# Kernel tuning notes

Measured on AMD Instinct MI355X. Metric: run time of the kernel, lower is better.

Reference implementation:

```python
import jax, jax.numpy as jnp
import numpy as np

N_STEPS = 3000  # hardcoded in the original forward loop


def setup_inputs() -> dict:
    return {
        "starting_value": jnp.float32(0.0),
        "rate": jnp.float32(1.0),
        "non_decision_time": jnp.float32(0.0),
        "threshold": jnp.float32(1.0),
        "noise": jnp.float32(1.0),
        "time_step_size": jnp.float32(0.01),
        "num_walkers": 1048576,
    }


def reference(starting_value, rate, non_decision_time, threshold, noise,
              time_step_size, num_walkers):
    # torch.normal(mean=rate*dt*active, std=noise*active):
    # inactive walkers get std=0, mean=0 -> dw == 0 exactly.
    # Equivalent: dw = active * (rate*dt + noise * z), z ~ N(0,1).
    sqrt_dt = jnp.sqrt(time_step_size)
    particle0 = jnp.zeros((num_walkers,), jnp.float32) + starting_value
    rts0 = jnp.zeros((num_walkers,), jnp.float32)
    active0 = jnp.ones((num_walkers,), jnp.bool_)

    keys = jax.random.split(jax.random.key(0), N_STEPS)

    def step(carry, k):
        particle, rts, active = carry
        a = active.astype(jnp.float32)
        z = jax.random.normal(k, (num_walkers,), jnp.float32)
        dw = (rate * time_step_size + noise * z) * a
        particle = particle + dw * sqrt_dt
        rts = rts + a
        active = jnp.abs(particle) < threshold
        return (particle, rts, active), None

    (particle, rts, _), _ = jax.lax.scan(step, (particle0, rts0, active0), keys)

    rts = non_decision_time + rts * time_step_size
    decisions = jnp.where(particle <= -threshold, 0.0, 1.0).astype(jnp.float32)
    return rts, decisions
```

## Files before the change

kernel.cpp:

```cpp
#include <hip/hip_runtime.h>
#include <math.h>

#define NSTEPS 3000
#define NWALK  1048576
#define BLOCK  256
#define NBD    (NWALK / BLOCK)
#define NDENSE 6
#define CHUNK  64
#define NBT    4096
#define NKEYS  3072

#define MAD(a, b, c) __fmaf_rn((a), (b), (c))

__device__ uint2    g_list[2][NWALK];
__device__ uint32_t g_cnt[16];
__device__ uint2    g_keys[NKEYS];

__device__ __forceinline__ void tf2x32(uint32_t k0, uint32_t k1,
                                       uint32_t x0, uint32_t x1,
                                       uint32_t& o0, uint32_t& o1) {
  uint32_t ks2 = k0 ^ k1 ^ 0x1BD11BDAu;
  x0 += k0; x1 += k1;
#define TFR(r) { x0 += x1; x1 = (x1 << r) | (x1 >> (32 - r)); x1 ^= x0; }
  TFR(13) TFR(15) TFR(26) TFR(6)
  x0 += k1;  x1 += ks2 + 1u;
  TFR(17) TFR(29) TFR(16) TFR(24)
  x0 += ks2; x1 += k0 + 2u;
  TFR(13) TFR(15) TFR(26) TFR(6)
  x0 += k0;  x1 += k1 + 3u;
  TFR(17) TFR(29) TFR(16) TFR(24)
  x0 += k1;  x1 += ks2 + 4u;
  TFR(13) TFR(15) TFR(26) TFR(6)
  x0 += ks2; x1 += k0 + 5u;
#undef TFR
  o0 = x0; o1 = x1;
}

__global__ void init_kernel() {
  int t = blockIdx.x * 256 + threadIdx.x;
  uint32_t a, b;
  tf2x32(0u, 0u, 0u, (uint32_t)t, a, b);
  g_keys[t] = make_uint2(a, b);
  if (blockIdx.x == 0 && threadIdx.x < 16) g_cnt[threadIdx.x] = 0u;
}

__device__ __forceinline__ float xla_cpu_log_f32(float s) {
  uint32_t bits = __float_as_uint(s);
  int emm0 = (int)(bits >> 23) - 0x7f;
  float e = __fadd_rn((float)emm0, 1.0f);
  float m = __uint_as_float((bits & 0x007fffffu) | 0x3f000000u);
  bool mlt = m < 0.70710677f;
  float tmp = mlt ? m : 0.0f;
  float x = __fsub_rn(m, 1.0f);
  e = __fsub_rn(e, mlt ? 1.0f : 0.0f);
  x = __fadd_rn(x, tmp);
  float x2 = __fmul_rn(x, x);
  float x3 = __fmul_rn(x2, x);
  float y, y1, y2;
  y  = MAD(7.0376836292e-2f,  x, -1.1514610310e-1f);
  y1 = MAD(-1.2420140846e-1f, x,  1.4249322787e-1f);
  y2 = MAD(2.0000714765e-1f,  x, -2.4999993993e-1f);
  y  = MAD(y,  x,  1.1676998740e-1f);
  y1 = MAD(y1, x, -1.6668057665e-1f);
  y2 = MAD(y2, x,  3.3333331174e-1f);
  y  = MAD(y, x3, y1);
  y  = MAD(y, x3, y2);
  y  = __fmul_rn(y, x3);
  y  = MAD(e, -2.12194440e-4f, y);
  x  = MAD(x2, -0.5f, x);
  x  = __fadd_rn(x, y);
  x  = MAD(e, 0.693359375f, x);
  return x;
}

__device__ __forceinline__ float xla_erfinv_f32(float x) {
  float s = __fmul_rn(__fsub_rn(1.0f, x), __fadd_rn(1.0f, x));
  float w = -xla_cpu_log_f32(s);
  float p;
  if (w < 5.0f) {
    float v = __fsub_rn(w, 2.5f);
    p = 2.81022636e-08f;
    p = MAD(p, v, 3.43273939e-07f);
    p = MAD(p, v, -3.5233877e-06f);
    p = MAD(p, v, -4.39150654e-06f);
    p = MAD(p, v, 0.00021858087f);
    p = MAD(p, v, -0.00125372503f);
    p = MAD(p, v, -0.00417768164f);
    p = MAD(p, v, 0.246640727f);
    p = MAD(p, v, 1.50140941f);
  } else {
    float v = __fsub_rn(__fsqrt_rn(w), 3.0f);
    p = -0.000200214257f;
    p = MAD(p, v, 0.000100950558f);
    p = MAD(p, v, 0.00134934322f);
    p = MAD(p, v, -0.00367342844f);
    p = MAD(p, v, 0.00573950773f);
    p = MAD(p, v, -0.0076224613f);
    p = MAD(p, v, 0.00943887047f);
    p = MAD(p, v, 1.00167406f);
    p = MAD(p, v, 2.83297682f);
  }
  return __fmul_rn(p, x);
}

__device__ __forceinline__ float normal_from_bits(uint32_t bits) {
  const float MINVAL = __uint_as_float(0xBF7FFFFFu);
  float f = __uint_as_float((bits >> 9) | 0x3F800000u) - 1.0f;
  float u = MAD(f, 2.0f, MINVAL);
  u = fmaxf(MINVAL, u);
  const float SQRT2 = __uint_as_float(0x3FB504F3u);
  return __fmul_rn(SQRT2, xla_erfinv_f32(u));
}

template<int R>
__device__ __forceinline__
void ddm_round_body(const float* __restrict__ sv_p, const float* __restrict__ rate_p,
                    const float* __restrict__ ndt_p, const float* __restrict__ thr_p,
                    const float* __restrict__ noise_p, const float* __restrict__ dt_p,
                    const int* __restrict__ nw_p, float* __restrict__ out) {
  constexpr int t0 = R * CHUNK;
  int nw = *nw_p;
  uint32_t count = (R == 0) ? (uint32_t)nw : g_cnt[R];
  if (blockIdx.x * BLOCK >= count) return;

  __shared__ uint2    skeys[CHUNK];
  __shared__ uint32_t s_woff[BLOCK / 64];
  __shared__ uint32_t s_base;
  if (threadIdx.x < CHUNK) {
    uint32_t a, b;
    tf2x32(0u, 0u, 0u, (uint32_t)(t0 + threadIdx.x), a, b);
    skeys[threadIdx.x] = make_uint2(a, b);
  }
  __syncthreads();

  uint32_t slot = blockIdx.x * BLOCK + threadIdx.x;
  bool alive = slot < count;
  float sv = *sv_p, rate = *rate_p, ndt = *ndt_p, thr = *thr_p,
        noise = *noise_p, dt = *dt_p;
  float rate_dt = __fmul_rn(rate, dt);
  float sqrt_dt = __fsqrt_rn(dt);
  int lane = threadIdx.x & 63;
  int wv = threadIdx.x >> 6;

  int i = 0; float p = 0.0f;
  if (alive) {
    if (R == 0) { i = (int)slot; p = __fadd_rn(0.0f, sv); }
    else { uint2 e = g_list[R & 1][slot]; i = (int)e.x; p = __uint_as_float(e.y); }
  }

  int death_s = -1;
  #pragma clang loop unroll(disable)
  for (int c = 0; c < CHUNK / 16; ++c) {
    #pragma unroll
    for (int j = 0; j < 16; ++j) {
      int s = c * 16 + j;
      if (alive) {
        uint2 k = skeys[s];
        uint32_t b1, b2;
        tf2x32(k.x, k.y, 0u, (uint32_t)i, b1, b2);
        float z = normal_from_bits(b1 ^ b2);
        p = __fadd_rn(p, __fmul_rn(__fadd_rn(rate_dt, __fmul_rn(noise, z)), sqrt_dt));
        if (!(fabsf(p) < thr)) { death_s = s; alive = false; }
      }
    }
  }
  if (death_s >= 0) {
    float rts = (float)(t0 + death_s + 1);
    out[i] = __fadd_rn(ndt, __fmul_rn(rts, dt));
    out[nw + i] = (p <= -thr) ? 0.0f : 1.0f;
  }

  uint64_t m = __ballot(alive);
  if (lane == 0) s_woff[wv] = (uint32_t)__popcll((unsigned long long)m);
  __syncthreads();
  if (threadIdx.x == 0) {
    uint32_t tot = 0;
    #pragma unroll
    for (int w = 0; w < BLOCK / 64; ++w) {
      uint32_t c = s_woff[w]; s_woff[w] = tot; tot += c;
    }
    s_base = tot ? atomicAdd(&g_cnt[R + 1], tot) : 0u;
  }
  __syncthreads();
  if (alive) {
    uint32_t pos = s_base + s_woff[wv] +
                   (uint32_t)__popcll((unsigned long long)(m & ((1ull << lane) - 1ull)));
    g_list[(R + 1) & 1][pos] = make_uint2((uint32_t)i, __float_as_uint(p));
  }
}

#define ARGS (const float* __restrict__ sv, const float* __restrict__ rate,   \
              const float* __restrict__ ndt, const float* __restrict__ thr,   \
              const float* __restrict__ noise, const float* __restrict__ dt,  \
              const int* __restrict__ nw, float* __restrict__ out)
#define DEFROUND(NAME, R)                                                     \
  __global__ __launch_bounds__(BLOCK) void NAME ARGS {                        \
    ddm_round_body<R>(sv, rate, ndt, thr, noise, dt, nw, out);                \
  }
DEFROUND(ddm_r0, 0)   DEFROUND(ddm_r1, 1)   DEFROUND(ddm_r2, 2)
DEFROUND(ddm_r3, 3)   DEFROUND(ddm_r4, 4)   DEFROUND(ddm_r5, 5)
#undef DEFROUND
#undef ARGS

__device__ __forceinline__ float rdlane_f(float v, int j) {
  return __uint_as_float((uint32_t)__builtin_amdgcn_readlane((int)__float_as_uint(v), j));
}

__global__ __launch_bounds__(BLOCK)
void ddm_tail(const float* __restrict__ sv_p, const float* __restrict__ rate_p,
              const float* __restrict__ ndt_p, const float* __restrict__ thr_p,
              const float* __restrict__ noise_p, const float* __restrict__ dt_p,
              const int* __restrict__ nw_p, float* __restrict__ out,
              int round, int t0) {
  int nw = *nw_p;
  float rate = *rate_p, ndt = *ndt_p, thr = *thr_p,
        noise = *noise_p, dt = *dt_p;
  float rate_dt = __fmul_rn(rate, dt);
  float sqrt_dt = __fsqrt_rn(dt);

  int lane = threadIdx.x & 63;
  uint32_t wave = blockIdx.x * (BLOCK / 64) + (threadIdx.x >> 6);
  uint32_t nwaves = gridDim.x * (BLOCK / 64);
  uint32_t count = g_cnt[round];

  for (uint32_t k = wave; k < count; k += nwaves) {
    uint2 e = g_list[round & 1][k];
    int i = (int)e.x;
    float p = __uint_as_float(e.y);
    int t = t0;
    int rts_i = NSTEPS;
    bool done = false;
    while (!done) {
      int valid = NSTEPS - t; if (valid > 64) valid = 64;
      int tl = t + (lane < valid ? lane : valid - 1);
      uint2 kk = g_keys[tl];
      uint32_t b1, b2;
      tf2x32(kk.x, kk.y, 0u, (uint32_t)i, b1, b2);
      float z = normal_from_bits(b1 ^ b2);
      float q = __fmul_rn(__fadd_rn(rate_dt, __fmul_rn(noise, z)), sqrt_dt);

      if (valid == 64) {
        float s0 = p, mx0 = 0.0f, mx1 = 0.0f, mx2 = 0.0f, mx3 = 0.0f;
        #pragma unroll
        for (int j = 0; j < 16; ++j) {
          p = __fadd_rn(p, rdlane_f(q, j));  mx0 = fmaxf(mx0, fabsf(p));
        }
        float s1 = p;
        #pragma unroll
        for (int j = 16; j < 32; ++j) {
          p = __fadd_rn(p, rdlane_f(q, j));  mx1 = fmaxf(mx1, fabsf(p));
        }
        float s2 = p;
        #pragma unroll
        for (int j = 32; j < 48; ++j) {
          p = __fadd_rn(p, rdlane_f(q, j));  mx2 = fmaxf(mx2, fabsf(p));
        }
        float s3 = p;
        #pragma unroll
        for (int j = 48; j < 64; ++j) {
          p = __fadd_rn(p, rdlane_f(q, j));  mx3 = fmaxf(mx3, fabsf(p));
        }
        if (fmaxf(fmaxf(mx0, mx1), fmaxf(mx2, mx3)) >= thr) {
          float pr; int jb;
          if      (mx0 >= thr) { pr = s0; jb = 0;  }
          else if (mx1 >= thr) { pr = s1; jb = 16; }
          else if (mx2 >= thr) { pr = s2; jb = 32; }
          else                 { pr = s3; jb = 48; }
          for (int j = 0; j < 16; ++j) {
            pr = __fadd_rn(pr, rdlane_f(q, jb + j));
            if (!(fabsf(pr) < thr)) {
              rts_i = t + jb + j + 1; p = pr; done = true; break;
            }
          }
        } else {
          t += 64;
          if (t >= NSTEPS) done = true;
        }
      } else {
        for (int j = 0; j < valid; ++j) {
          float qj = rdlane_f(q, j);
          p = __fadd_rn(p, qj);
          if (!(fabsf(p) < thr)) { rts_i = t + j + 1; done = true; break; }
        }
        if (!done) {
          t += valid;
          if (t >= NSTEPS) done = true;
        }
      }
    }
    if (lane == 0) {
      out[i] = __fadd_rn(ndt, __fmul_rn((float)rts_i, dt));
      out[nw + i] = (p <= -thr) ? 0.0f : 1.0f;
    }
  }
}

extern "C" void kernel_launch(void* const* d_in, const int* in_sizes, int n_in,
                              void* d_out, int out_size, void* d_ws, size_t ws_size,
                              hipStream_t stream) {
  const float* sv    = (const float*)d_in[0];
  const float* rate  = (const float*)d_in[1];
  const float* ndt   = (const float*)d_in[2];
  const float* thr   = (const float*)d_in[3];
  const float* noise = (const float*)d_in[4];
  const float* dt    = (const float*)d_in[5];
  const int*   nw    = (const int*)d_in[6];
  float* out = (float*)d_out;

  init_kernel<<<NKEYS / 256, 256, 0, stream>>>();
  ddm_r0<<<NBD, BLOCK, 0, stream>>>(sv, rate, ndt, thr, noise, dt, nw, out);
  ddm_r1<<<NBD, BLOCK, 0, stream>>>(sv, rate, ndt, thr, noise, dt, nw, out);
  ddm_r2<<<NBD, BLOCK, 0, stream>>>(sv, rate, ndt, thr, noise, dt, nw, out);
  ddm_r3<<<NBD, BLOCK, 0, stream>>>(sv, rate, ndt, thr, noise, dt, nw, out);
  ddm_r4<<<NBD, BLOCK, 0, stream>>>(sv, rate, ndt, thr, noise, dt, nw, out);
  ddm_r5<<<NBD, BLOCK, 0, stream>>>(sv, rate, ndt, thr, noise, dt, nw, out);
  ddm_tail<<<NBT, BLOCK, 0, stream>>>(sv, rate, ndt, thr, noise, dt, nw, out,
                                      NDENSE, NDENSE * CHUNK);
}
```

Measured before the change: 521.7 us.

## Compact surviving walkers within block every 16 steps using shared-memory exchange

Round kernels now use 1024-thread blocks and, every 16 steps inside a chunk, write out finished walkers, then compact the still-active walkers to the front of the block through a shared-memory exchange. Dead lanes no longer sit idle through the rest of the chunk, and whole waves can exit early once their block runs out of active walkers. The cost is extra barriers and shared-memory traffic per sub-chunk, plus larger blocks, which may lower occupancy. The tail kernel stays at 256 threads.

```diff
diff --git a/kernel.cpp b/kernel.cpp
--- a/kernel.cpp
+++ b/kernel.cpp
@@ -3,10 +3,11 @@
 
 #define NSTEPS 3000
 #define NWALK  1048576
-#define BLOCK  256
+#define BLOCK  1024
 #define NBD    (NWALK / BLOCK)
 #define NDENSE 6
 #define CHUNK  64
+#define NWAVES (BLOCK / 64)
 #define NBT    4096
 #define NKEYS  3072
 
@@ -124,7 +125,8 @@
   if (blockIdx.x * BLOCK >= count) return;
 
   __shared__ uint2    skeys[CHUNK];
-  __shared__ uint32_t s_woff[BLOCK / 64];
+  __shared__ uint2    s_exch[BLOCK];
+  __shared__ uint32_t s_woff[NWAVES];
   __shared__ uint32_t s_base;
   if (threadIdx.x < CHUNK) {
     uint32_t a, b;
@@ -151,6 +153,36 @@
   int death_s = -1;
   #pragma clang loop unroll(disable)
   for (int c = 0; c < CHUNK / 16; ++c) {
+    if (c > 0) {
+      if (death_s >= 0) {
+        float rts = (float)(t0 + death_s + 1);
+        out[i] = __fadd_rn(ndt, __fmul_rn(rts, dt));
+        out[nw + i] = (p <= -thr) ? 0.0f : 1.0f;
+        death_s = -1;
+      }
+      uint64_t m = __ballot(alive);
+      if (lane == 0) s_woff[wv] = (uint32_t)__popcll((unsigned long long)m);
+      __syncthreads();
+      uint32_t total = 0, base = 0;
+      #pragma unroll
+      for (int w = 0; w < NWAVES; ++w) {
+        uint32_t cw = s_woff[w];
+        if (w < wv) base += cw;
+        total += cw;
+      }
+      if (total == 0) break;
+      if (alive) {
+        uint32_t pos = base +
+            (uint32_t)__popcll((unsigned long long)(m & ((1ull << lane) - 1ull)));
+        s_exch[pos] = make_uint2((uint32_t)i, __float_as_uint(p));
+      }
+      __syncthreads();
+      alive = threadIdx.x < total;
+      if (alive) {
+        uint2 e = s_exch[threadIdx.x];
+        i = (int)e.x; p = __uint_as_float(e.y);
+      }
+    }
     #pragma unroll
     for (int j = 0; j < 16; ++j) {
       int s = c * 16 + j;
@@ -176,7 +208,7 @@
   if (threadIdx.x == 0) {
     uint32_t tot = 0;
     #pragma unroll
-    for (int w = 0; w < BLOCK / 64; ++w) {
+    for (int w = 0; w < NWAVES; ++w) {
       uint32_t c = s_woff[w]; s_woff[w] = tot; tot += c;
     }
     s_base = tot ? atomicAdd(&g_cnt[R + 1], tot) : 0u;
@@ -206,7 +238,7 @@
   return __uint_as_float((uint32_t)__builtin_amdgcn_readlane((int)__float_as_uint(v), j));
 }
 
-__global__ __launch_bounds__(BLOCK)
+__global__ __launch_bounds__(256)
 void ddm_tail(const float* __restrict__ sv_p, const float* __restrict__ rate_p,
               const float* __restrict__ ndt_p, const float* __restrict__ thr_p,
               const float* __restrict__ noise_p, const float* __restrict__ dt_p,
@@ -219,8 +251,8 @@
   float sqrt_dt = __fsqrt_rn(dt);
 
   int lane = threadIdx.x & 63;
-  uint32_t wave = blockIdx.x * (BLOCK / 64) + (threadIdx.x >> 6);
-  uint32_t nwaves = gridDim.x * (BLOCK / 64);
+  uint32_t wave = blockIdx.x * (256 / 64) + (threadIdx.x >> 6);
+  uint32_t nwaves = gridDim.x * (256 / 64);
   uint32_t count = g_cnt[round];
 
   for (uint32_t k = wave; k < count; k += nwaves) {
@@ -314,6 +346,6 @@
   ddm_r3<<<NBD, BLOCK, 0, stream>>>(sv, rate, ndt, thr, noise, dt, nw, out);
   ddm_r4<<<NBD, BLOCK, 0, stream>>>(sv, rate, ndt, thr, noise, dt, nw, out);
   ddm_r5<<<NBD, BLOCK, 0, stream>>>(sv, rate, ndt, thr, noise, dt, nw, out);
-  ddm_tail<<<NBT, BLOCK, 0, stream>>>(sv, rate, ndt, thr, noise, dt, nw, out,
-                                      NDENSE, NDENSE * CHUNK);
-}
+  ddm_tail<<<NBT, 256, 0, stream>>>(sv, rate, ndt, thr, noise, dt, nw, out,
+                                    NDENSE, NDENSE * CHUNK);
+}
```

Result: slower. 605.2 us (+16.0%).
